# Kernel optimization log

Hardware: AMD Instinct MI355X
Metric: run time of the kernel (lower is better)

Reference implementation:

```python
import jax, jax.numpy as jnp
import numpy as np

B, S, HID, NH = 4, 2048, 1024, 16
HD = HID // NH  # head_dim = 64


def setup_inputs() -> dict:
    key = jax.random.key(0)
    ks = jax.random.split(key, 5)
    scale = 0.02
    return {
        "hidden_states": jax.random.normal(ks[0], (B, S, HID), dtype=jnp.float32),
        "attention_mask": jnp.zeros((B, 1, 1, S), dtype=jnp.float32),
        "Wq": jax.random.normal(ks[1], (HID, HID), dtype=jnp.float32) * scale,
        "bq": jnp.zeros((HID,), dtype=jnp.float32),
        "Wk": jax.random.normal(ks[2], (HID, HID), dtype=jnp.float32) * scale,
        "bk": jnp.zeros((HID,), dtype=jnp.float32),
        "Wv": jax.random.normal(ks[3], (HID, HID), dtype=jnp.float32) * scale,
        "bv": jnp.zeros((HID,), dtype=jnp.float32),
    }


def _split_heads(x):
    # [B, S, HID] -> [B, NH, S, HD]
    b, s, _ = x.shape
    return x.reshape(b, s, NH, HD).transpose(0, 2, 1, 3)


def reference(hidden_states, attention_mask, Wq, bq, Wk, bk, Wv, bv):
    # Linear projections (torch Linear: x @ W.T + b)
    q = _split_heads(hidden_states @ Wq.T + bq)
    k = _split_heads(hidden_states @ Wk.T + bk)
    v = _split_heads(hidden_states @ Wv.T + bv)

    # scores: [B, NH, S, S]
    scores = jnp.einsum("bhqd,bhkd->bhqk", q, k) / jnp.sqrt(jnp.float32(HD))
    scores = scores + attention_mask  # additive mask, broadcast over heads/query
    weights = jax.nn.softmax(scores, axis=-1)
    # dropout prob = 0 (inference), head_mask = None

    context = jnp.einsum("bhqk,bhkd->bhqd", weights, v)
    # [B, NH, S, HD] -> [B, S, HID]
    context = context.transpose(0, 2, 1, 3).reshape(hidden_states.shape[0], hidden_states.shape[1], HID)
    return context
```

## Files before the change

kernel.cpp:

```cpp
#include <hip/hip_runtime.h>
#include <stdint.h>


typedef float f32x4 __attribute__((ext_vector_type(4)));
typedef float f32x16 __attribute__((ext_vector_type(16)));
typedef __bf16 bf16x8 __attribute__((ext_vector_type(8)));
typedef unsigned short ushort_t;
typedef uint32_t u32;

#define MFMA16(a, b, c) __builtin_amdgcn_mfma_f32_16x16x32_bf16(a, b, c, 0, 0, 0)
#define MFMA32(a, b, c) __builtin_amdgcn_mfma_f32_32x32x16_bf16(a, b, c, 0, 0, 0)

__device__ __forceinline__ ushort_t f2b(float f) {
    union { float f; uint32_t u; } x{f};
    uint32_t r = (x.u + 0x7fffu + ((x.u >> 16) & 1u)) >> 16;
    return (ushort_t)r;
}

__device__ __forceinline__ float fexp2(float x) {
#if __has_builtin(__builtin_amdgcn_exp2f)
    return __builtin_amdgcn_exp2f(x);
#else
    return exp2f(x);
#endif
}

__device__ __forceinline__ u32 pkpair(float e, float o) {
    union { float f; u32 u; } xe{e}, xo{o};
    return __builtin_amdgcn_perm(xo.u, xe.u, 0x07060302u);
}

__device__ __forceinline__ bf16x8 mk8(u32 a, u32 b, u32 c, u32 d) {
    union { u32 u[4]; bf16x8 v; } x;
    x.u[0] = a; x.u[1] = b; x.u[2] = c; x.u[3] = d;
    return x.v;
}

__device__ __forceinline__ void gld_lds16(const void* g, void* l) {
    __builtin_amdgcn_global_load_lds(
        (const __attribute__((address_space(1))) unsigned int*)g,
        (__attribute__((address_space(3))) unsigned int*)l, 16, 0, 0);
}

__global__ __launch_bounds__(256) void convert_k(
    const float* __restrict__ hs, const float* __restrict__ wq,
    const float* __restrict__ wk, const float* __restrict__ wv,
    ushort_t* __restrict__ hs_b, ushort_t* __restrict__ w_b) {
    size_t c = (size_t)blockIdx.x * 256 + threadIdx.x;
    size_t i = c * 8;
    const size_t NHS = (size_t)8192 * 1024;
    const float* src;
    ushort_t* dst;
    if (i < NHS) { src = hs + i; dst = hs_b + i; }
    else {
        size_t j = i - NHS;
        int w = (int)(j >> 20);
        size_t o = j & ((1u << 20) - 1);
        src = (w == 0 ? wq : (w == 1 ? wk : wv)) + o;
        dst = w_b + ((size_t)w << 20) + o;
    }
    float4 a = *(const float4*)src;
    float4 b = *(const float4*)(src + 4);
    uint32_t p0 = (uint32_t)f2b(a.x) | ((uint32_t)f2b(a.y) << 16);
    uint32_t p1 = (uint32_t)f2b(a.z) | ((uint32_t)f2b(a.w) << 16);
    uint32_t p2 = (uint32_t)f2b(b.x) | ((uint32_t)f2b(b.y) << 16);
    uint32_t p3 = (uint32_t)f2b(b.z) | ((uint32_t)f2b(b.w) << 16);
    uint4 v{p0, p1, p2, p3};
    *(uint4*)dst = v;
}

__global__ __launch_bounds__(256, 4) void qkv_gemm(
    const ushort_t* __restrict__ Ab, const ushort_t* __restrict__ Wb,
    const float* __restrict__ bq, const float* __restrict__ bk,
    const float* __restrict__ bv, ushort_t* __restrict__ q_ws,
    ushort_t* __restrict__ k_ws, ushort_t* __restrict__ vt_ws) {
    __shared__ __align__(16) char smem_raw[128 * 136 * 2];
    ushort_t* At = (ushort_t*)smem_raw;
    ushort_t* Bt = At + 128 * 64;
    ushort_t* Ct = (ushort_t*)smem_raw;
    int which = blockIdx.z;
    const ushort_t* W = Wb + ((size_t)which << 20);
    int m0 = blockIdx.y * 128, n0 = blockIdx.x * 128;
    int t = threadIdx.x, lane = t & 63, wave = t >> 6;
    int quad = lane >> 4, l16 = lane & 15;
    int wr = (wave >> 1) * 64, wc = (wave & 1) * 64;
    f32x4 acc[4][4] = {};
    for (int k0 = 0; k0 < 1024; k0 += 64) {
        for (int r = 0; r < 4; r++) {
            int idx = r * 256 + t;
            int row = idx >> 3, co = (idx & 7) * 8;
            gld_lds16(Ab + (size_t)(m0 + row) * 1024 + k0 + co, At + idx * 8);
            gld_lds16(W + (size_t)(n0 + row) * 1024 + k0 + co, Bt + idx * 8);
        }
        asm volatile("s_waitcnt vmcnt(0)" ::: "memory");
        __syncthreads();
        for (int kk = 0; kk < 2; kk++) {
            bf16x8 af[4], bf[4];
            for (int i = 0; i < 4; i++)
                af[i] = *(const bf16x8*)(At + (wr + i * 16 + l16) * 64 + kk * 32 + quad * 8);
            for (int j = 0; j < 4; j++)
                bf[j] = *(const bf16x8*)(Bt + (wc + j * 16 + l16) * 64 + kk * 32 + quad * 8);
            for (int i = 0; i < 4; i++)
                for (int j = 0; j < 4; j++)
                    acc[i][j] = MFMA16(af[i], bf[j], acc[i][j]);
        }
        __syncthreads();
    }
    const float* bias = which == 0 ? bq : (which == 1 ? bk : bv);
    float sc = which == 0 ? (0.125f * 1.44269504f) : 1.0f;
    if (which == 2) {
        for (int j = 0; j < 4; j++) {
            float bias_v = bias[n0 + wc + j * 16 + l16];
            for (int i = 0; i < 4; i++) {
                ushort4 pk;
                pk.x = f2b(acc[i][j].x + bias_v);
                pk.y = f2b(acc[i][j].y + bias_v);
                pk.z = f2b(acc[i][j].z + bias_v);
                pk.w = f2b(acc[i][j].w + bias_v);
                *(ushort4*)(Ct + (wc + j * 16 + l16) * 136 + wr + i * 16 + quad * 4) = pk;
            }
        }
    } else {
        for (int j = 0; j < 4; j++) {
            float bias_v = bias[n0 + wc + j * 16 + l16];
            int col = wc + j * 16 + l16;
            for (int i = 0; i < 4; i++) {
                int rb = wr + i * 16 + quad * 4;
                Ct[(rb + 0) * 136 + col] = f2b((acc[i][j].x + bias_v) * sc);
                Ct[(rb + 1) * 136 + col] = f2b((acc[i][j].y + bias_v) * sc);
                Ct[(rb + 2) * 136 + col] = f2b((acc[i][j].z + bias_v) * sc);
                Ct[(rb + 3) * 136 + col] = f2b((acc[i][j].w + bias_v) * sc);
            }
        }
    }
    __syncthreads();
    for (int r = 0; r < 8; r++) {
        int idx = r * 256 + t;
        int row = idx >> 4, c8 = (idx & 15) * 8;
        uint4 val = *(const uint4*)(Ct + row * 136 + c8);
        if (which == 2) {
            int col = n0 + row, h = col >> 6, d = col & 63;
            int tok = m0 + c8, b = tok >> 11, s = tok & 2047;
            *(uint4*)(vt_ws + ((size_t)(b * 16 + h) * 64 + d) * 2048 + s) = val;
        } else {
            int tok = m0 + row, b = tok >> 11, s = tok & 2047;
            int col = n0 + c8, h = col >> 6, d = col & 63;
            ushort_t* base = which == 0 ? q_ws : k_ws;
            *(uint4*)(base + ((size_t)(b * 16 + h) * 2048 + s) * 64 + d) = val;
        }
    }
}

__global__ __launch_bounds__(256, 2) void attn_k(
    const ushort_t* __restrict__ q_ws, const ushort_t* __restrict__ k_ws,
    const ushort_t* __restrict__ vt_ws, const float* __restrict__ mask,
    float* __restrict__ out) {
    __shared__ __align__(16) char smraw[33280];
    ushort_t* Kl = (ushort_t*)smraw;
    ushort_t* Vtl = Kl + 64 * 64;
    float* Ow = (float*)smraw;

    int bh = blockIdx.y, b = bh >> 4, h = bh & 15;
    int q0 = blockIdx.x * 256;
    int t = threadIdx.x, lane = t & 63, w = t >> 6;
    int l31 = lane & 31, hi = lane >> 5;
    bool h0 = (hi == 0);
    const ushort_t* Q = q_ws + (size_t)bh * 2048 * 64;
    const ushort_t* K = k_ws + (size_t)bh * 2048 * 64;
    const ushort_t* Vt = vt_ws + (size_t)bh * 64 * 2048;
    const float* mrow = mask + b * 2048;

    bf16x8 qf[2][4];
#pragma unroll
    for (int qg = 0; qg < 2; qg++)
#pragma unroll
        for (int cs = 0; cs < 4; cs++)
            qf[qg][cs] = *(const bf16x8*)(
                Q + (size_t)(q0 + w * 64 + qg * 32 + l31) * 64 + cs * 16 + hi * 8);
    int co[4];
#pragma unroll
    for (int cs = 0; cs < 4; cs++) co[cs] = ((cs * 2 + hi) ^ (l31 & 7)) * 8;

    f32x16 o00 = {}, o01 = {}, o10 = {}, o11 = {};
    float rs0 = 0.f, rs1 = 0.f;

    for (int t0 = 0; t0 < 2048; t0 += 64) {
#pragma unroll
        for (int it = 0; it < 2; it++) {
            int idx = it * 256 + t;
            int row = idx >> 3, ch = idx & 7;
            int sch = (ch ^ (row & 7)) * 8;
            gld_lds16(K + (size_t)(t0 + row) * 64 + sch, Kl + idx * 8);
            gld_lds16(Vt + (size_t)row * 2048 + t0 + sch, Vtl + idx * 8);
        }
        asm volatile("s_waitcnt vmcnt(0)" ::: "memory");
        __syncthreads();
        f32x16 s00 = {}, s01 = {}, s10 = {}, s11 = {};
#pragma unroll
        for (int cs = 0; cs < 4; cs++) {
            bf16x8 k0 = *(const bf16x8*)(Kl + l31 * 64 + co[cs]);
            bf16x8 k1 = *(const bf16x8*)(Kl + (32 + l31) * 64 + co[cs]);
            s00 = MFMA32(k0, qf[0][cs], s00);
            s01 = MFMA32(k1, qf[0][cs], s01);
            s10 = MFMA32(k0, qf[1][cs], s10);
            s11 = MFMA32(k1, qf[1][cs], s11);
        }
        bf16x8 pfr[2][4];
#pragma unroll
        for (int qg = 0; qg < 2; qg++) {
            const f32x16& sa = qg ? s10 : s00;
            const f32x16& sb = qg ? s11 : s01;
            u32 pa[8], pb[8];
            float rst = 0.f;
#pragma unroll
            for (int i = 0; i < 4; i++) {
                float4 bm = *(const float4*)(mrow + t0 + 8 * i + 4 * hi);
                float e0 = fexp2(fmaf(bm.x, 1.44269504f, sa[4 * i + 0]));
                float e1 = fexp2(fmaf(bm.y, 1.44269504f, sa[4 * i + 1]));
                float e2 = fexp2(fmaf(bm.z, 1.44269504f, sa[4 * i + 2]));
                float e3 = fexp2(fmaf(bm.w, 1.44269504f, sa[4 * i + 3]));
                rst += (e0 + e1) + (e2 + e3);
                pa[2 * i] = pkpair(e0, e1);
                pa[2 * i + 1] = pkpair(e2, e3);
            }
#pragma unroll
            for (int i = 0; i < 4; i++) {
                float4 bm = *(const float4*)(mrow + t0 + 32 + 8 * i + 4 * hi);
                float e0 = fexp2(fmaf(bm.x, 1.44269504f, sb[4 * i + 0]));
                float e1 = fexp2(fmaf(bm.y, 1.44269504f, sb[4 * i + 1]));
                float e2 = fexp2(fmaf(bm.z, 1.44269504f, sb[4 * i + 2]));
                float e3 = fexp2(fmaf(bm.w, 1.44269504f, sb[4 * i + 3]));
                rst += (e0 + e1) + (e2 + e3);
                pb[2 * i] = pkpair(e0, e1);
                pb[2 * i + 1] = pkpair(e2, e3);
            }
            if (qg == 0) rs0 += rst; else rs1 += rst;
#pragma unroll
            for (int g = 0; g < 4; g++) {
                const u32* aa = (g < 2) ? pa : pb;
                int base = (g & 1) * 4;
                u32 y0 = h0 ? aa[base + 2] : aa[base + 0];
                u32 y1 = h0 ? aa[base + 3] : aa[base + 1];
                u32 sy0 = (u32)__shfl_xor((int)y0, 32, 64);
                u32 sy1 = (u32)__shfl_xor((int)y1, 32, 64);
                pfr[qg][g] = mk8(h0 ? aa[base + 0] : sy0, h0 ? aa[base + 1] : sy1,
                                 h0 ? sy0 : aa[base + 2], h0 ? sy1 : aa[base + 3]);
            }
        }
#pragma unroll
        for (int cs = 0; cs < 4; cs++) {
            bf16x8 v0 = *(const bf16x8*)(Vtl + l31 * 64 + co[cs]);
            bf16x8 v1 = *(const bf16x8*)(Vtl + (32 + l31) * 64 + co[cs]);
            o00 = MFMA32(v0, pfr[0][cs], o00);
            o01 = MFMA32(v1, pfr[0][cs], o01);
            o10 = MFMA32(v0, pfr[1][cs], o10);
            o11 = MFMA32(v1, pfr[1][cs], o11);
        }
        __syncthreads();
    }
    rs0 += __shfl_xor(rs0, 32, 64);
    rs1 += __shfl_xor(rs1, 32, 64);
    float inv0 = 1.f / rs0, inv1 = 1.f / rs1;
#pragma unroll
    for (int qg = 0; qg < 2; qg++) {
        float inv = qg ? inv1 : inv0;
        const f32x16& a0 = qg ? o10 : o00;
        const f32x16& a1 = qg ? o11 : o01;
#pragma unroll
        for (int g = 0; g < 4; g++) {
            f32x4 c0, c1;
#pragma unroll
            for (int r = 0; r < 4; r++) {
                c0[r] = a0[4 * g + r] * inv;
                c1[r] = a1[4 * g + r] * inv;
            }
            *(f32x4*)(Ow + (w * 32 + l31) * 65 + 8 * g + 4 * hi) = c0;
            *(f32x4*)(Ow + (w * 32 + l31) * 65 + 32 + 8 * g + 4 * hi) = c1;
        }
        __syncthreads();
#pragma unroll
        for (int cc = 0; cc < 8; cc++) {
            int c = cc * 256 + t;
            int row = c >> 4, seg = (c & 15) * 4;
            f32x4 vv = *(const f32x4*)(Ow + row * 65 + seg);
            int ql = (row >> 5) * 64 + qg * 32 + (row & 31);
            *(f32x4*)(out + ((size_t)(b * 2048 + q0 + ql)) * 1024 + h * 64 + seg) = vv;
        }
        __syncthreads();
    }
}

extern "C" void kernel_launch(void* const* d_in, const int* in_sizes, int n_in,
                              void* d_out, int out_size, void* d_ws, size_t ws_size,
                              hipStream_t stream) {
    const float* hs = (const float*)d_in[0];
    const float* mask = (const float*)d_in[1];
    const float* wq = (const float*)d_in[2];
    const float* bq = (const float*)d_in[3];
    const float* wk = (const float*)d_in[4];
    const float* bk = (const float*)d_in[5];
    const float* wv = (const float*)d_in[6];
    const float* bv = (const float*)d_in[7];
    float* out = (float*)d_out;
    char* ws = (char*)d_ws;
    ushort_t* hs_b = (ushort_t*)ws;
    ushort_t* w_b = (ushort_t*)(ws + 16777216);
    ushort_t* q_ws = (ushort_t*)(ws + 23068672);
    ushort_t* k_ws = (ushort_t*)(ws + 39845888);
    ushort_t* vt_ws = (ushort_t*)(ws + 56623104);

    convert_k<<<5632, 256, 0, stream>>>(hs, wq, wk, wv, hs_b, w_b);
    qkv_gemm<<<dim3(8, 64, 3), 256, 0, stream>>>(hs_b, w_b, bq, bk, bv, q_ws, k_ws, vt_ws);
    attn_k<<<dim3(8, 64), 256, 0, stream>>>(q_ws, k_ws, vt_ws, mask, out);
}
```

Measured before the change: 258.7 us.

## Double-buffer K/V tiles in LDS and stage pre-scaled mask in shared memory

The attention kernel now keeps two LDS buffers for the K and V^T tiles. It issues the global-to-LDS loads for the next key tile before computing on the current one, so the load latency overlaps the MFMA and softmax work instead of stalling on a full wait each iteration. The additive mask row is also copied once into LDS, already multiplied by log2(e). That turns each per-tile global float4 mask load plus FMA into an LDS read plus an add. LDS use per block grows to 40 KB. Correctness of the overlap depends on the end-of-loop barrier also waiting for the outstanding vector-memory loads.

Result: no change. 257.8 us (-0.4%).

```diff
diff --git a/kernel.cpp b/kernel.cpp
--- a/kernel.cpp
+++ b/kernel.cpp
@@ -155,9 +155,8 @@
     const ushort_t* __restrict__ q_ws, const ushort_t* __restrict__ k_ws,
     const ushort_t* __restrict__ vt_ws, const float* __restrict__ mask,
     float* __restrict__ out) {
-    __shared__ __align__(16) char smraw[33280];
-    ushort_t* Kl = (ushort_t*)smraw;
-    ushort_t* Vtl = Kl + 64 * 64;
+    __shared__ __align__(16) char smraw[40960];
+    float* Ml = (float*)(smraw + 32768);
     float* Ow = (float*)smraw;
 
     int bh = blockIdx.y, b = bh >> 4, h = bh & 15;
@@ -168,7 +167,11 @@
     const ushort_t* Q = q_ws + (size_t)bh * 2048 * 64;
     const ushort_t* K = k_ws + (size_t)bh * 2048 * 64;
     const ushort_t* Vt = vt_ws + (size_t)bh * 64 * 2048;
-    const float* mrow = mask + b * 2048;
+
+    for (int r = 0; r < 8; r++) {
+        int i = r * 256 + t;
+        Ml[i] = mask[b * 2048 + i] * 1.44269504f;
+    }
 
     bf16x8 qf[2][4];
 #pragma unroll
@@ -184,17 +187,27 @@
     f32x16 o00 = {}, o01 = {}, o10 = {}, o11 = {};
     float rs0 = 0.f, rs1 = 0.f;
 
-    for (int t0 = 0; t0 < 2048; t0 += 64) {
+    auto stage = [&](int bufi, int t0) {
+        ushort_t* Klb = (ushort_t*)(smraw + bufi * 16384);
+        ushort_t* Vtlb = Klb + 4096;
 #pragma unroll
         for (int it = 0; it < 2; it++) {
             int idx = it * 256 + t;
             int row = idx >> 3, ch = idx & 7;
             int sch = (ch ^ (row & 7)) * 8;
-            gld_lds16(K + (size_t)(t0 + row) * 64 + sch, Kl + idx * 8);
-            gld_lds16(Vt + (size_t)row * 2048 + t0 + sch, Vtl + idx * 8);
-        }
-        asm volatile("s_waitcnt vmcnt(0)" ::: "memory");
-        __syncthreads();
+            gld_lds16(K + (size_t)(t0 + row) * 64 + sch, Klb + idx * 8);
+            gld_lds16(Vt + (size_t)row * 2048 + t0 + sch, Vtlb + idx * 8);
+        }
+    };
+
+    stage(0, 0);
+    asm volatile("s_waitcnt vmcnt(0)" ::: "memory");
+    __syncthreads();
+    int buf = 0;
+    for (int t0 = 0; t0 < 2048; t0 += 64) {
+        if (t0 + 64 < 2048) stage(buf ^ 1, t0 + 64);
+        const ushort_t* Kl = (const ushort_t*)(smraw + buf * 16384);
+        const ushort_t* Vtl = Kl + 4096;
         f32x16 s00 = {}, s01 = {}, s10 = {}, s11 = {};
 #pragma unroll
         for (int cs = 0; cs < 4; cs++) {
@@ -214,22 +227,22 @@
             float rst = 0.f;
 #pragma unroll
             for (int i = 0; i < 4; i++) {
-                float4 bm = *(const float4*)(mrow + t0 + 8 * i + 4 * hi);
-                float e0 = fexp2(fmaf(bm.x, 1.44269504f, sa[4 * i + 0]));
-                float e1 = fexp2(fmaf(bm.y, 1.44269504f, sa[4 * i + 1]));
-                float e2 = fexp2(fmaf(bm.z, 1.44269504f, sa[4 * i + 2]));
-                float e3 = fexp2(fmaf(bm.w, 1.44269504f, sa[4 * i + 3]));
+                f32x4 bm = *(const f32x4*)(Ml + t0 + 8 * i + 4 * hi);
+                float e0 = fexp2(sa[4 * i + 0] + bm[0]);
+                float e1 = fexp2(sa[4 * i + 1] + bm[1]);
+                float e2 = fexp2(sa[4 * i + 2] + bm[2]);
+                float e3 = fexp2(sa[4 * i + 3] + bm[3]);
                 rst += (e0 + e1) + (e2 + e3);
                 pa[2 * i] = pkpair(e0, e1);
                 pa[2 * i + 1] = pkpair(e2, e3);
             }
 #pragma unroll
             for (int i = 0; i < 4; i++) {
-                float4 bm = *(const float4*)(mrow + t0 + 32 + 8 * i + 4 * hi);
-                float e0 = fexp2(fmaf(bm.x, 1.44269504f, sb[4 * i + 0]));
-                float e1 = fexp2(fmaf(bm.y, 1.44269504f, sb[4 * i + 1]));
-                float e2 = fexp2(fmaf(bm.z, 1.44269504f, sb[4 * i + 2]));
-                float e3 = fexp2(fmaf(bm.w, 1.44269504f, sb[4 * i + 3]));
+                f32x4 bm = *(const f32x4*)(Ml + t0 + 32 + 8 * i + 4 * hi);
+                float e0 = fexp2(sb[4 * i + 0] + bm[0]);
+                float e1 = fexp2(sb[4 * i + 1] + bm[1]);
+                float e2 = fexp2(sb[4 * i + 2] + bm[2]);
+                float e3 = fexp2(sb[4 * i + 3] + bm[3]);
                 rst += (e0 + e1) + (e2 + e3);
                 pb[2 * i] = pkpair(e0, e1);
                 pb[2 * i + 1] = pkpair(e2, e3);
@@ -257,6 +270,7 @@
             o11 = MFMA32(v1, pfr[1][cs], o11);
         }
         __syncthreads();
+        buf ^= 1;
     }
     rs0 += __shfl_xor(rs0, 32, 64);
     rs1 += __shfl_xor(rs1, 32, 64);
```

## Load K and V fragments directly from global memory, dropping LDS staging

Applied to the files above, without the earlier changes.

The attention kernel no longer stages each 64-token K/Vt tile through shared memory with async global-to-LDS copies and barriers. Each wave now loads its MFMA operand fragments straight from global memory into registers, relying on L1/L2 caching since all four waves read the same tile. This removes the __syncthreads pair and the LDS traffic per iteration, and shrinks LDS to the output staging buffer. In exchange it gives up cross-wave data sharing and raises global/cache traffic and load latency exposure.

Measured after the change: 304.7 us. 1.18x slower.

```diff
diff --git a/kernel.cpp b/kernel.cpp
--- a/kernel.cpp
+++ b/kernel.cpp
@@ -155,10 +155,7 @@
     const ushort_t* __restrict__ q_ws, const ushort_t* __restrict__ k_ws,
     const ushort_t* __restrict__ vt_ws, const float* __restrict__ mask,
     float* __restrict__ out) {
-    __shared__ __align__(16) char smraw[33280];
-    ushort_t* Kl = (ushort_t*)smraw;
-    ushort_t* Vtl = Kl + 64 * 64;
-    float* Ow = (float*)smraw;
+    __shared__ __align__(16) float Ow[128 * 65];
 
     int bh = blockIdx.y, b = bh >> 4, h = bh & 15;
     int q0 = blockIdx.x * 256;
@@ -177,33 +174,35 @@
         for (int cs = 0; cs < 4; cs++)
             qf[qg][cs] = *(const bf16x8*)(
                 Q + (size_t)(q0 + w * 64 + qg * 32 + l31) * 64 + cs * 16 + hi * 8);
-    int co[4];
-#pragma unroll
-    for (int cs = 0; cs < 4; cs++) co[cs] = ((cs * 2 + hi) ^ (l31 & 7)) * 8;
 
     f32x16 o00 = {}, o01 = {}, o10 = {}, o11 = {};
     float rs0 = 0.f, rs1 = 0.f;
 
+    const ushort_t* Krow0 = K + (size_t)l31 * 64 + hi * 8;
+    const ushort_t* Krow1 = K + (size_t)(32 + l31) * 64 + hi * 8;
+    const ushort_t* Vrow0 = Vt + (size_t)l31 * 2048 + hi * 8;
+    const ushort_t* Vrow1 = Vt + (size_t)(32 + l31) * 2048 + hi * 8;
+
     for (int t0 = 0; t0 < 2048; t0 += 64) {
-#pragma unroll
-        for (int it = 0; it < 2; it++) {
-            int idx = it * 256 + t;
-            int row = idx >> 3, ch = idx & 7;
-            int sch = (ch ^ (row & 7)) * 8;
-            gld_lds16(K + (size_t)(t0 + row) * 64 + sch, Kl + idx * 8);
-            gld_lds16(Vt + (size_t)row * 2048 + t0 + sch, Vtl + idx * 8);
-        }
-        asm volatile("s_waitcnt vmcnt(0)" ::: "memory");
-        __syncthreads();
+        bf16x8 k0[4], k1[4];
+#pragma unroll
+        for (int cs = 0; cs < 4; cs++) {
+            k0[cs] = *(const bf16x8*)(Krow0 + (size_t)t0 * 64 + cs * 16);
+            k1[cs] = *(const bf16x8*)(Krow1 + (size_t)t0 * 64 + cs * 16);
+        }
         f32x16 s00 = {}, s01 = {}, s10 = {}, s11 = {};
 #pragma unroll
         for (int cs = 0; cs < 4; cs++) {
-            bf16x8 k0 = *(const bf16x8*)(Kl + l31 * 64 + co[cs]);
-            bf16x8 k1 = *(const bf16x8*)(Kl + (32 + l31) * 64 + co[cs]);
-            s00 = MFMA32(k0, qf[0][cs], s00);
-            s01 = MFMA32(k1, qf[0][cs], s01);
-            s10 = MFMA32(k0, qf[1][cs], s10);
-            s11 = MFMA32(k1, qf[1][cs], s11);
+            s00 = MFMA32(k0[cs], qf[0][cs], s00);
+            s01 = MFMA32(k1[cs], qf[0][cs], s01);
+            s10 = MFMA32(k0[cs], qf[1][cs], s10);
+            s11 = MFMA32(k1[cs], qf[1][cs], s11);
+        }
+        bf16x8 v0[4], v1[4];
+#pragma unroll
+        for (int cs = 0; cs < 4; cs++) {
+            v0[cs] = *(const bf16x8*)(Vrow0 + t0 + cs * 16);
+            v1[cs] = *(const bf16x8*)(Vrow1 + t0 + cs * 16);
         }
         bf16x8 pfr[2][4];
 #pragma unroll
@@ -249,14 +248,11 @@
         }
 #pragma unroll
         for (int cs = 0; cs < 4; cs++) {
-            bf16x8 v0 = *(const bf16x8*)(Vtl + l31 * 64 + co[cs]);
-            bf16x8 v1 = *(const bf16x8*)(Vtl + (32 + l31) * 64 + co[cs]);
-            o00 = MFMA32(v0, pfr[0][cs], o00);
-            o01 = MFMA32(v1, pfr[0][cs], o01);
-            o10 = MFMA32(v0, pfr[1][cs], o10);
-            o11 = MFMA32(v1, pfr[1][cs], o11);
-        }
-        __syncthreads();
+            o00 = MFMA32(v0[cs], pfr[0][cs], o00);
+            o01 = MFMA32(v1[cs], pfr[0][cs], o01);
+            o10 = MFMA32(v0[cs], pfr[1][cs], o10);
+            o11 = MFMA32(v1[cs], pfr[1][cs], o11);
+        }
     }
     rs0 += __shfl_xor(rs0, 32, 64);
     rs1 += __shfl_xor(rs1, 32, 64);
```
